# Performance work log

Hardware: AMD Instinct MI355X
Metric: run time of the kernel (lower is better)

## Reference

```python
import jax, jax.numpy as jnp
import numpy as np

EMBED_DIM = 1024
NUM_HEAD = 16
HEAD_DIM = EMBED_DIM // NUM_HEAD


def _linear_params(key, in_dim, out_dim):
    kw, kb = jax.random.split(key)
    bound = 1.0 / np.sqrt(in_dim)
    W = jax.random.uniform(kw, (out_dim, in_dim), minval=-bound, maxval=bound, dtype=jnp.float32)
    b = jax.random.uniform(kb, (out_dim,), minval=-bound, maxval=bound, dtype=jnp.float32)
    return W, b


def setup_inputs() -> dict:
    key = jax.random.key(0)
    ks = jax.random.split(key, 7)
    N, S, E = 2, 2048, EMBED_DIM
    k = jax.random.normal(ks[0], (N, S, E), dtype=jnp.float32)
    q = jax.random.normal(ks[1], (N, S, E), dtype=jnp.float32)
    v = jax.random.normal(ks[2], (N, S, E), dtype=jnp.float32)
    Wk, bk = _linear_params(ks[3], E, E)
    Wq, bq = _linear_params(ks[4], E, E)
    Wv, bv = _linear_params(ks[5], E, E)
    Wo, bo = _linear_params(ks[6], E, E)
    return {"key": k, "query": q, "value": v,
            "Wk": Wk, "bk": bk, "Wq": Wq, "bq": bq,
            "Wv": Wv, "bv": bv, "Wo": Wo, "bo": bo}


def reference(key, query, value, Wk, bk, Wq, bq, Wv, bv, Wo, bo):
    N, S_in, E = key.shape
    S_out = query.shape[1]
    H, D = NUM_HEAD, HEAD_DIM
    # projections (torch Linear: x @ W.T + b), split heads -> [N, H, S, D]
    k = (key @ Wk.T + bk).reshape(N, S_in, H, D).transpose(0, 2, 1, 3)
    q = (query @ Wq.T + bq).reshape(N, S_out, H, D).transpose(0, 2, 1, 3)
    v = (value @ Wv.T + bv).reshape(N, S_in, H, D).transpose(0, 2, 1, 3)
    # unfused attention: full [N,H,S_out,S_in] score matrix, scale, softmax
    weight = jnp.einsum("nhqd,nhkd->nhqk", q, k) / jnp.sqrt(jnp.float32(D))
    weight = jax.nn.softmax(weight, axis=-1)
    attn = jnp.einsum("nhqk,nhkd->nhqd", weight, v)  # [N,H,S_out,D]
    attn = attn.transpose(0, 2, 1, 3).reshape(N, S_out, E)
    return attn @ Wo.T + bo
```

## Files before the change

### kernel.cpp

```cpp
#include <hip/hip_runtime.h>

constexpr int E  = 1024;
constexpr int NH = 16;
constexpr int HD = 64;
constexpr int S  = 2048;
constexpr int NB = 2;
constexpr int M  = NB * S;

typedef unsigned short u16;
typedef _Float16 f16;
typedef __attribute__((ext_vector_type(8))) _Float16 h8v;
typedef __attribute__((ext_vector_type(2))) __fp16 hp2v;
typedef __attribute__((ext_vector_type(4))) float f4v;

__device__ __forceinline__ f4v mfmaH(h8v a, h8v b, f4v c) {
    return __builtin_amdgcn_mfma_f32_16x16x32_f16(a, b, c, 0, 0, 0);
}
__device__ __forceinline__ u16 f16bits(float x) {
    union { f16 h; u16 u; } t; t.h = (f16)x; return t.u;
}
__device__ __forceinline__ unsigned pkrtz(float a, float b) {
    union { hp2v h; unsigned u; } t;
    t.h = __builtin_amdgcn_cvt_pkrtz(a, b);
    return t.u;
}
typedef const __attribute__((address_space(1))) void gvoid;
typedef __attribute__((address_space(3))) void lvoid;
__device__ __forceinline__ void load_lds16(const u16* g, u16* l) {
    __builtin_amdgcn_global_load_lds((gvoid*)g, (lvoid*)l, 16, 0, 0);
}

__global__ __launch_bounds__(256)
void cvt_f16(const float* __restrict__ q, const float* __restrict__ k,
             const float* __restrict__ v,
             const float* __restrict__ wq, const float* __restrict__ wk,
             const float* __restrict__ wv, const float* __restrict__ wo,
             u16* __restrict__ out)
{
    const size_t ME = (size_t)M * E, EE = (size_t)E * E;
    const int z = blockIdx.y;
    const float* src = (z == 0) ? q : (z == 1) ? k : (z == 2) ? v
                     : (z == 3) ? wq : (z == 4) ? wk : (z == 5) ? wv : wo;
    const size_t len = (z < 3) ? ME : EE;
    u16* dst = out + ((z < 3) ? (size_t)z * ME : 3 * ME + (size_t)(z - 3) * EE);
    for (size_t i = ((size_t)blockIdx.x * 256 + threadIdx.x) * 8; i < len;
         i += (size_t)gridDim.x * 256 * 8) {
        float4 a = *reinterpret_cast<const float4*>(src + i);
        float4 b = *reinterpret_cast<const float4*>(src + i + 4);
        h8v o;
        o[0] = (f16)a.x; o[1] = (f16)a.y; o[2] = (f16)a.z; o[3] = (f16)a.w;
        o[4] = (f16)b.x; o[5] = (f16)b.y; o[6] = (f16)b.z; o[7] = (f16)b.w;
        *reinterpret_cast<h8v*>(dst + i) = o;
    }
}

__device__ __forceinline__ void gemm16_core(const u16* __restrict__ A,
                                            const u16* __restrict__ W,
                                            int bm, int bn, u16* lds, f4v acc[4][4])
{
    const int tid  = threadIdx.x;
    const int lane = tid & 63;
    const int wid  = tid >> 6;
    const int g = lane >> 4, c = lane & 15;
    const int wr = wid >> 1, wc = wid & 1;
    const int lrow = lane >> 3;
    const int lslot = lane & 7;
    const int sslot = lslot ^ lrow;

    for (int k0 = 0; k0 < E; k0 += 64) {
        #pragma unroll
        for (int i = 0; i < 4; ++i) {
            int rbase = wid * 32 + i * 8;
            load_lds16(A + (size_t)(bm + rbase + lrow) * E + k0 + (sslot << 3),
                       &lds[rbase * 64]);
            load_lds16(W + (size_t)(bn + rbase + lrow) * E + k0 + (sslot << 3),
                       &lds[8192 + rbase * 64]);
        }
        __syncthreads();

        h8v a[4][2];
        #pragma unroll
        for (int mf = 0; mf < 4; ++mf) {
            int row = wr * 64 + mf * 16 + c;
            #pragma unroll
            for (int ks = 0; ks < 2; ++ks)
                a[mf][ks] = *reinterpret_cast<h8v*>(
                    &lds[row * 64 + ((((ks << 2) | g) ^ (c & 7)) << 3)]);
        }
        #pragma unroll
        for (int nf = 0; nf < 4; ++nf) {
            int row = wc * 64 + nf * 16 + c;
            #pragma unroll
            for (int ks = 0; ks < 2; ++ks) {
                h8v b = *reinterpret_cast<h8v*>(
                    &lds[8192 + row * 64 + ((((ks << 2) | g) ^ (c & 7)) << 3)]);
                #pragma unroll
                for (int mf = 0; mf < 4; ++mf)
                    acc[mf][nf] = mfmaH(a[mf][ks], b, acc[mf][nf]);
            }
        }
        __syncthreads();
    }
}

__global__ __launch_bounds__(256, 3)
void qkv_gemm(const u16* __restrict__ qf, const u16* __restrict__ kf,
              const u16* __restrict__ vf,
              const u16* __restrict__ wqf, const u16* __restrict__ wkf,
              const u16* __restrict__ wvf,
              const float* __restrict__ bq, const float* __restrict__ bk,
              const float* __restrict__ bv,
              u16* __restrict__ Qattn, u16* __restrict__ KV, float scaleQ)
{
    __shared__ __align__(16) u16 lds[16384];
    const int z = blockIdx.z;
    const u16* A = (z == 0) ? qf : (z == 1) ? kf : vf;
    const u16* W = (z == 0) ? wqf : (z == 1) ? wkf : wvf;
    const float* bias = (z == 0) ? bq : (z == 1) ? bk : bv;
    const float scl = (z == 0) ? scaleQ : 1.0f;
    const int bm = blockIdx.x * 128, bn = blockIdx.y * 128;

    f4v acc[4][4];
    #pragma unroll
    for (int a = 0; a < 4; ++a)
        #pragma unroll
        for (int b = 0; b < 4; ++b) acc[a][b] = (f4v){0.f, 0.f, 0.f, 0.f};

    gemm16_core(A, W, bm, bn, lds, acc);

    const int lane = threadIdx.x & 63;
    const int g = lane >> 4, c = lane & 15;
    const int wid = threadIdx.x >> 6;
    const int wr = wid >> 1, wc = wid & 1;
    float bcol[4];
    #pragma unroll
    for (int nf = 0; nf < 4; ++nf) bcol[nf] = bias[bn + wc * 64 + nf * 16 + c];

    #pragma unroll
    for (int mf = 0; mf < 4; ++mf)
        #pragma unroll
        for (int r = 0; r < 4; ++r) {
            int m  = bm + wr * 64 + mf * 16 + g * 4 + r;
            int nb = m >> 11, sp = m & (S - 1);
            #pragma unroll
            for (int nf = 0; nf < 4; ++nf) {
                int ncol = bn + wc * 64 + nf * 16 + c;
                int h = ncol >> 6, d = ncol & 63;
                int bh_ = nb * NH + h;
                u16 hb = f16bits((acc[mf][nf][r] + bcol[nf]) * scl);
                if (z == 0) {
                    Qattn[((size_t)bh_ * S + sp) * HD + d] = hb;
                } else if (z == 1) {
                    int t = sp >> 6, kk = (sp >> 4) & 3, cc = sp & 15;
                    int ds = d >> 5, gg = (d >> 3) & 3, j = d & 7;
                    KV[((size_t)bh_ * 32 + t) * 8192 +
                       ((size_t)((kk * 2 + ds) * 64 + gg * 16 + cc)) * 8 + j] = hb;
                } else {
                    int t = sp >> 6, rem = sp & 63;
                    int s2 = rem >> 5, bb = (rem >> 4) & 1, gg = (rem >> 2) & 3, a2 = rem & 3;
                    int j = 4 * bb + a2;
                    int df = d >> 4, cc = d & 15;
                    KV[((size_t)bh_ * 32 + t) * 8192 + 4096 +
                       ((size_t)((df * 2 + s2) * 64 + gg * 16 + cc)) * 8 + j] = hb;
                }
            }
        }
}

__global__ __launch_bounds__(256, 3)
void out_gemm(const u16* __restrict__ A, const u16* __restrict__ W,
              const float* __restrict__ bias, float* __restrict__ C)
{
    __shared__ __align__(16) u16 lds[16384];
    const int bm = blockIdx.x * 128, bn = blockIdx.y * 128;
    f4v acc[4][4];
    #pragma unroll
    for (int a = 0; a < 4; ++a)
        #pragma unroll
        for (int b = 0; b < 4; ++b) acc[a][b] = (f4v){0.f, 0.f, 0.f, 0.f};

    gemm16_core(A, W, bm, bn, lds, acc);

    const int lane = threadIdx.x & 63;
    const int g = lane >> 4, c = lane & 15;
    const int wid = threadIdx.x >> 6;
    const int wr = wid >> 1, wc = wid & 1;
    float bcol[4];
    #pragma unroll
    for (int nf = 0; nf < 4; ++nf) bcol[nf] = bias[bn + wc * 64 + nf * 16 + c];

    #pragma unroll
    for (int mf = 0; mf < 4; ++mf)
        #pragma unroll
        for (int r = 0; r < 4; ++r) {
            int m = bm + wr * 64 + mf * 16 + g * 4 + r;
            float* crow = &C[(size_t)m * E + bn + wc * 64];
            #pragma unroll
            for (int nf = 0; nf < 4; ++nf)
                crow[nf * 16 + c] = acc[mf][nf][r] + bcol[nf];
        }
}

__global__ __launch_bounds__(256, 4)
void attn_mfma(const u16* __restrict__ Qf, const u16* __restrict__ KV,
               u16* __restrict__ Out)
{
    __shared__ __align__(16) u16 lds[16384];
    const int tid  = threadIdx.x;
    const int lane = tid & 63;
    const int wid  = tid >> 6;
    const int g = lane >> 4, c = lane & 15;
    const int dlin = blockIdx.x;
    const int idx  = dlin >> 3;
    const int bh = (dlin & 7) * 4 + (idx >> 5);
    const int qc = idx & 31;
    const int n = bh >> 4, h = bh & 15;
    const int q0 = qc * 64 + wid * 16;
    const u16* kvb = KV + (size_t)bh * 32 * 8192;
    const f4v zero4 = {0.f, 0.f, 0.f, 0.f};

    h8v Qb[2];
    #pragma unroll
    for (int ds = 0; ds < 2; ++ds)
        Qb[ds] = *reinterpret_cast<const h8v*>(
            &Qf[((size_t)bh * S + q0 + c) * HD + ds * 32 + g * 8]);

    h8v ones;
    #pragma unroll
    for (int i = 0; i < 8; ++i) ones[i] = (f16)1.0f;

    f4v oacc[4];
    #pragma unroll
    for (int df = 0; df < 4; ++df) oacc[df] = zero4;
    f4v lacc = zero4;

    {
        const u16* src = kvb + wid * 2048 + lane * 8;
        u16* dst = &lds[wid * 2048];
        #pragma unroll
        for (int i = 0; i < 4; ++i) load_lds16(src + i * 512, dst + i * 512);
        src += 8192;
        dst += 8192;
        #pragma unroll
        for (int i = 0; i < 4; ++i) load_lds16(src + i * 512, dst + i * 512);
    }

    int cur = 0;
    #define ATTN_TILE_BODY(BT)                                                  \
    {                                                                           \
        const u16* Bt = (BT);                                                   \
                                    \
        h8v vh[4][2];                                                           \
        _Pragma("unroll")                                                       \
        for (int df = 0; df < 4; ++df)                                          \
            _Pragma("unroll")                                                   \
            for (int s2 = 0; s2 < 2; ++s2)                                      \
                vh[df][s2] = *reinterpret_cast<const h8v*>(                     \
                    &Bt[4096 + ((size_t)((df * 2 + s2) * 64 + lane)) * 8]);     \
        f4v sc[4];                                                              \
        _Pragma("unroll")                                                       \
        for (int kf = 0; kf < 4; ++kf) sc[kf] = zero4;                          \
        __builtin_amdgcn_s_setprio(1);                                          \
        _Pragma("unroll")                                                       \
        for (int kf = 0; kf < 4; ++kf) {                                        \
            _Pragma("unroll")                                                   \
            for (int ds = 0; ds < 2; ++ds) {                                    \
                h8v kh = *reinterpret_cast<const h8v*>(                         \
                    &Bt[((size_t)((kf * 2 + ds) * 64 + lane)) * 8]);            \
                sc[kf] = mfmaH(kh, Qb[ds], sc[kf]);                             \
            }                                                                   \
        }                                                                       \
        __builtin_amdgcn_s_setprio(0);                                          \
        unsigned pkh[4][2];                                                     \
        _Pragma("unroll")                                                       \
        for (int kf = 0; kf < 4; ++kf) {                                        \
            _Pragma("unroll")                                                   \
            for (int r = 0; r < 4; ++r) sc[kf][r] = exp2f(sc[kf][r]);           \
            pkh[kf][0] = pkrtz(sc[kf][0], sc[kf][1]);                           \
            pkh[kf][1] = pkrtz(sc[kf][2], sc[kf][3]);                           \
        }                                                                       \
        h8v pah[2];                                                             \
        _Pragma("unroll")                                                       \
        for (int s2 = 0; s2 < 2; ++s2) {                                        \
            union { h8v v; unsigned u[4]; } th;                                 \
            th.u[0] = pkh[2 * s2][0];     th.u[1] = pkh[2 * s2][1];             \
            th.u[2] = pkh[2 * s2 + 1][0]; th.u[3] = pkh[2 * s2 + 1][1];         \
            pah[s2] = th.v;                                                     \
        }                                                                       \
        __builtin_amdgcn_s_setprio(1);                                          \
        lacc = mfmaH(pah[0], ones, lacc);                                       \
        lacc = mfmaH(pah[1], ones, lacc);                                       \
        _Pragma("unroll")                                                       \
        for (int df = 0; df < 4; ++df)                                          \
            _Pragma("unroll")                                                   \
            for (int s2 = 0; s2 < 2; ++s2)                                      \
                oacc[df] = mfmaH(pah[s2], vh[df][s2], oacc[df]);                \
        __builtin_amdgcn_s_setprio(0);                                          \
    }

    for (int t = 0; t < 31; ++t) {
        asm volatile("s_waitcnt vmcnt(4)" ::: "memory");
        __builtin_amdgcn_s_barrier();
        ATTN_TILE_BODY(&lds[cur * 8192]);
        __builtin_amdgcn_s_barrier();
        if (t < 30) {
            const u16* src = kvb + (size_t)(t + 2) * 8192 + wid * 2048 + lane * 8;
            u16* dst = &lds[cur * 8192 + wid * 2048];
            #pragma unroll
            for (int i = 0; i < 4; ++i) load_lds16(src + i * 512, dst + i * 512);
        }
        cur ^= 1;
    }
    asm volatile("s_waitcnt vmcnt(0)" ::: "memory");
    __builtin_amdgcn_s_barrier();
    ATTN_TILE_BODY(&lds[cur * 8192]);
    #undef ATTN_TILE_BODY

    #pragma unroll
    for (int r = 0; r < 4; ++r) {
        float linv = 1.0f / lacc[r];
        int q = q0 + g * 4 + r;
        size_t ob = ((size_t)n * S + q) * E + h * HD;
        #pragma unroll
        for (int df = 0; df < 4; ++df)
            Out[ob + df * 16 + c] = f16bits(oacc[df][r] * linv);
    }
}

extern "C" void kernel_launch(void* const* d_in, const int* in_sizes, int n_in,
                              void* d_out, int out_size, void* d_ws, size_t ws_size,
                              hipStream_t stream)
{
    const float* key   = (const float*)d_in[0];
    const float* query = (const float*)d_in[1];
    const float* value = (const float*)d_in[2];
    const float* Wk    = (const float*)d_in[3];
    const float* bk    = (const float*)d_in[4];
    const float* Wq    = (const float*)d_in[5];
    const float* bq    = (const float*)d_in[6];
    const float* Wv    = (const float*)d_in[7];
    const float* bv    = (const float*)d_in[8];
    const float* Wo    = (const float*)d_in[9];
    const float* bo    = (const float*)d_in[10];

    const size_t ME = (size_t)M * E, EE = (size_t)E * E;
    u16* ws16  = (u16*)d_ws;
    u16* qf16  = ws16;
    u16* kf16  = ws16 + ME;
    u16* vf16  = ws16 + 2 * ME;
    u16* wqf   = ws16 + 3 * ME;
    u16* wkf   = wqf + EE;
    u16* wvf   = wkf + EE;
    u16* wof   = wvf + EE;
    u16* Qattn = wof + EE;
    u16* KV    = Qattn + ME;
    u16* AoutH = ws16;

    const float SCALE_Q = 0.125f * 1.44269504088896340736f;

    cvt_f16<<<dim3(2048, 7), 256, 0, stream>>>(query, key, value, Wq, Wk, Wv, Wo, ws16);
    qkv_gemm<<<dim3(M / 128, E / 128, 3), 256, 0, stream>>>(
        qf16, kf16, vf16, wqf, wkf, wvf, bq, bk, bv, Qattn, KV, SCALE_Q);
    attn_mfma<<<dim3((S / 64) * NB * NH), 256, 0, stream>>>(Qattn, KV, AoutH);
    out_gemm<<<dim3(M / 128, E / 128), 256, 0, stream>>>(AoutH, wof, bo, (float*)d_out);
}
```

Baseline: 127.4 us.

## Process two query fragments per wave in attention with 128-thread blocks

The attention kernel now runs 2 waves per block instead of 4, and each wave handles 32 query rows (two 16-row fragments) that share the K and V fragments read from LDS. This halves the LDS reads per MFMA and doubles the per-wave share of the async KV tile loads. exp2f is swapped for raw v_exp_f32 inline asm, which skips any range handling. The cost is more registers per wave and fewer waves per block to hide latency, with launch bounds changed to (128, 2).

Result: faster. 116.3 us (-8.7%).

```diff
diff --git a/kernel.cpp b/kernel.cpp
--- a/kernel.cpp
+++ b/kernel.cpp
@@ -23,6 +23,11 @@
     union { hp2v h; unsigned u; } t;
     t.h = __builtin_amdgcn_cvt_pkrtz(a, b);
     return t.u;
+}
+__device__ __forceinline__ float fexp2(float x) {
+    float r;
+    asm("v_exp_f32 %0, %1" : "=v"(r) : "v"(x));
+    return r;
 }
 typedef const __attribute__((address_space(1))) void gvoid;
 typedef __attribute__((address_space(3))) void lvoid;
@@ -201,7 +206,7 @@
         }
 }
 
-__global__ __launch_bounds__(256, 4)
+__global__ __launch_bounds__(128, 2)
 void attn_mfma(const u16* __restrict__ Qf, const u16* __restrict__ KV,
                u16* __restrict__ Out)
 {
@@ -215,34 +220,35 @@
     const int bh = (dlin & 7) * 4 + (idx >> 5);
     const int qc = idx & 31;
     const int n = bh >> 4, h = bh & 15;
-    const int q0 = qc * 64 + wid * 16;
+    const int q0 = qc * 64 + wid * 32;
     const u16* kvb = KV + (size_t)bh * 32 * 8192;
     const f4v zero4 = {0.f, 0.f, 0.f, 0.f};
 
-    h8v Qb[2];
-    #pragma unroll
-    for (int ds = 0; ds < 2; ++ds)
-        Qb[ds] = *reinterpret_cast<const h8v*>(
-            &Qf[((size_t)bh * S + q0 + c) * HD + ds * 32 + g * 8]);
+    h8v Qb[2][2];
+    #pragma unroll
+    for (int qf = 0; qf < 2; ++qf)
+        #pragma unroll
+        for (int ds = 0; ds < 2; ++ds)
+            Qb[qf][ds] = *reinterpret_cast<const h8v*>(
+                &Qf[((size_t)bh * S + q0 + qf * 16 + c) * HD + ds * 32 + g * 8]);
 
     h8v ones;
     #pragma unroll
     for (int i = 0; i < 8; ++i) ones[i] = (f16)1.0f;
 
-    f4v oacc[4];
-    #pragma unroll
-    for (int df = 0; df < 4; ++df) oacc[df] = zero4;
-    f4v lacc = zero4;
-
-    {
-        const u16* src = kvb + wid * 2048 + lane * 8;
-        u16* dst = &lds[wid * 2048];
-        #pragma unroll
-        for (int i = 0; i < 4; ++i) load_lds16(src + i * 512, dst + i * 512);
-        src += 8192;
-        dst += 8192;
-        #pragma unroll
-        for (int i = 0; i < 4; ++i) load_lds16(src + i * 512, dst + i * 512);
+    f4v oacc[2][4];
+    #pragma unroll
+    for (int qf = 0; qf < 2; ++qf)
+        #pragma unroll
+        for (int df = 0; df < 4; ++df) oacc[qf][df] = zero4;
+    f4v lacc[2] = {zero4, zero4};
+
+    #pragma unroll
+    for (int tt = 0; tt < 2; ++tt) {
+        const u16* src = kvb + tt * 8192 + wid * 4096 + lane * 8;
+        u16* dst = &lds[tt * 8192 + wid * 4096];
+        #pragma unroll
+        for (int i = 0; i < 8; ++i) load_lds16(src + i * 512, dst + i * 512);
     }
 
     int cur = 0;
@@ -257,9 +263,11 @@
             for (int s2 = 0; s2 < 2; ++s2)                                      \
                 vh[df][s2] = *reinterpret_cast<const h8v*>(                     \
                     &Bt[4096 + ((size_t)((df * 2 + s2) * 64 + lane)) * 8]);     \
-        f4v sc[4];                                                              \
-        _Pragma("unroll")                                                       \
-        for (int kf = 0; kf < 4; ++kf) sc[kf] = zero4;                          \
+        f4v sc[2][4];                                                           \
+        _Pragma("unroll")                                                       \
+        for (int qf = 0; qf < 2; ++qf)                                          \
+            _Pragma("unroll")                                                   \
+            for (int kf = 0; kf < 4; ++kf) sc[qf][kf] = zero4;                  \
         __builtin_amdgcn_s_setprio(1);                                          \
         _Pragma("unroll")                                                       \
         for (int kf = 0; kf < 4; ++kf) {                                        \
@@ -267,47 +275,56 @@
             for (int ds = 0; ds < 2; ++ds) {                                    \
                 h8v kh = *reinterpret_cast<const h8v*>(                         \
                     &Bt[((size_t)((kf * 2 + ds) * 64 + lane)) * 8]);            \
-                sc[kf] = mfmaH(kh, Qb[ds], sc[kf]);                             \
+                _Pragma("unroll")                                               \
+                for (int qf = 0; qf < 2; ++qf)                                  \
+                    sc[qf][kf] = mfmaH(kh, Qb[qf][ds], sc[qf][kf]);             \
             }                                                                   \
         }                                                                       \
         __builtin_amdgcn_s_setprio(0);                                          \
-        unsigned pkh[4][2];                                                     \
-        _Pragma("unroll")                                                       \
-        for (int kf = 0; kf < 4; ++kf) {                                        \
-            _Pragma("unroll")                                                   \
-            for (int r = 0; r < 4; ++r) sc[kf][r] = exp2f(sc[kf][r]);           \
-            pkh[kf][0] = pkrtz(sc[kf][0], sc[kf][1]);                           \
-            pkh[kf][1] = pkrtz(sc[kf][2], sc[kf][3]);                           \
+        h8v pah[2][2];                                                          \
+        _Pragma("unroll")                                                       \
+        for (int qf = 0; qf < 2; ++qf)                                          \
+            _Pragma("unroll")                                                   \
+            for (int s2 = 0; s2 < 2; ++s2) {                                    \
+                union { h8v v; unsigned u[4]; } th;                             \
+                _Pragma("unroll")                                               \
+                for (int kfh = 0; kfh < 2; ++kfh) {                             \
+                    int kf = 2 * s2 + kfh;                                      \
+                    float p0 = fexp2(sc[qf][kf][0]);                            \
+                    float p1 = fexp2(sc[qf][kf][1]);                            \
+                    float p2 = fexp2(sc[qf][kf][2]);                            \
+                    float p3 = fexp2(sc[qf][kf][3]);                            \
+                    th.u[2 * kfh + 0] = pkrtz(p0, p1);                          \
+                    th.u[2 * kfh + 1] = pkrtz(p2, p3);                          \
+                }                                                               \
+                pah[qf][s2] = th.v;                                             \
+            }                                                                   \
+        __builtin_amdgcn_s_setprio(1);                                          \
+        _Pragma("unroll")                                                       \
+        for (int qf = 0; qf < 2; ++qf) {                                        \
+            lacc[qf] = mfmaH(pah[qf][0], ones, lacc[qf]);                       \
+            lacc[qf] = mfmaH(pah[qf][1], ones, lacc[qf]);                       \
         }                                                                       \
-        h8v pah[2];                                                             \
-        _Pragma("unroll")                                                       \
-        for (int s2 = 0; s2 < 2; ++s2) {                                        \
-            union { h8v v; unsigned u[4]; } th;                                 \
-            th.u[0] = pkh[2 * s2][0];     th.u[1] = pkh[2 * s2][1];             \
-            th.u[2] = pkh[2 * s2 + 1][0]; th.u[3] = pkh[2 * s2 + 1][1];         \
-            pah[s2] = th.v;                                                     \
-        }                                                                       \
-        __builtin_amdgcn_s_setprio(1);                                          \
-        lacc = mfmaH(pah[0], ones, lacc);                                       \
-        lacc = mfmaH(pah[1], ones, lacc);                                       \
         _Pragma("unroll")                                                       \
         for (int df = 0; df < 4; ++df)                                          \
             _Pragma("unroll")                                                   \
             for (int s2 = 0; s2 < 2; ++s2)                                      \
-                oacc[df] = mfmaH(pah[s2], vh[df][s2], oacc[df]);                \
+                _Pragma("unroll")                                               \
+                for (int qf = 0; qf < 2; ++qf)                                  \
+                    oacc[qf][df] = mfmaH(pah[qf][s2], vh[df][s2], oacc[qf][df]);\
         __builtin_amdgcn_s_setprio(0);                                          \
     }
 
     for (int t = 0; t < 31; ++t) {
-        asm volatile("s_waitcnt vmcnt(4)" ::: "memory");
+        asm volatile("s_waitcnt vmcnt(8)" ::: "memory");
         __builtin_amdgcn_s_barrier();
         ATTN_TILE_BODY(&lds[cur * 8192]);
         __builtin_amdgcn_s_barrier();
         if (t < 30) {
-            const u16* src = kvb + (size_t)(t + 2) * 8192 + wid * 2048 + lane * 8;
-            u16* dst = &lds[cur * 8192 + wid * 2048];
-            #pragma unroll
-            for (int i = 0; i < 4; ++i) load_lds16(src + i * 512, dst + i * 512);
+            const u16* src = kvb + (size_t)(t + 2) * 8192 + wid * 4096 + lane * 8;
+            u16* dst = &lds[cur * 8192 + wid * 4096];
+            #pragma unroll
+            for (int i = 0; i < 8; ++i) load_lds16(src + i * 512, dst + i * 512);
         }
         cur ^= 1;
     }
@@ -317,14 +334,16 @@
     #undef ATTN_TILE_BODY
 
     #pragma unroll
-    for (int r = 0; r < 4; ++r) {
-        float linv = 1.0f / lacc[r];
-        int q = q0 + g * 4 + r;
-        size_t ob = ((size_t)n * S + q) * E + h * HD;
-        #pragma unroll
-        for (int df = 0; df < 4; ++df)
-            Out[ob + df * 16 + c] = f16bits(oacc[df][r] * linv);
-    }
+    for (int qf = 0; qf < 2; ++qf)
+        #pragma unroll
+        for (int r = 0; r < 4; ++r) {
+            float linv = 1.0f / lacc[qf][r];
+            int q = q0 + qf * 16 + g * 4 + r;
+            size_t ob = ((size_t)n * S + q) * E + h * HD;
+            #pragma unroll
+            for (int df = 0; df < 4; ++df)
+                Out[ob + df * 16 + c] = f16bits(oacc[qf][df][r] * linv);
+        }
 }
 
 extern "C" void kernel_launch(void* const* d_in, const int* in_sizes, int n_in,
@@ -361,6 +380,6 @@
     cvt_f16<<<dim3(2048, 7), 256, 0, stream>>>(query, key, value, Wq, Wk, Wv, Wo, ws16);
     qkv_gemm<<<dim3(M / 128, E / 128, 3), 256, 0, stream>>>(
         qf16, kf16, vf16, wqf, wkf, wvf, bq, bk, bv, Qattn, KV, SCALE_Q);
-    attn_mfma<<<dim3((S / 64) * NB * NH), 256, 0, stream>>>(Qattn, KV, AoutH);
+    attn_mfma<<<dim3((S / 64) * NB * NH), 128, 0, stream>>>(Qattn, KV, AoutH);
     out_gemm<<<dim3(M / 128, E / 128), 256, 0, stream>>>(AoutH, wof, bo, (float*)d_out);
 }
```
